# Kernel optimization log

Hardware: AMD Instinct MI355X
Metric: run time of the kernel (lower is better)

## Reference

```python
import jax, jax.numpy as jnp
import numpy as np

B = 32
C = 768
NH = 12
HD = C // NH
P = 16
IMG = 224
G = IMG // P           # 14 patches per side
NP = G * G             # 196 patches
DEPTH = 12
PRUNE = [1, 1, 1, 1, 0.5, 0.5, 0.5, 0.5, 0.5, 0.5, 0.5, 0.5]
MOM = 0.5              # momentum for global class-attention update
TRADE = 0.5            # slow-fast tradeoff for placeholder token update
SCALE = HD ** -0.5
NCLS = 1000

def _ln(x, g, b, eps=1e-6):
    mu = jnp.mean(x, -1, keepdims=True)
    var = jnp.mean((x - mu) ** 2, -1, keepdims=True)
    return (x - mu) * jax.lax.rsqrt(var + eps) * g + b

def setup_inputs():
    key = jax.random.key(0)
    ks = iter(jax.random.split(key, 40))
    def rn(shape, s=0.02):
        return jax.random.normal(next(ks), shape, jnp.float32) * s
    return {
        'x_img': jax.random.normal(next(ks), (B, 3, IMG, IMG), jnp.float32),
        'cls_token': rn((1, 1, C)),
        'pos_embed': rn((1, NP + 1, C)),
        'patch_w': rn((3 * P * P, C)),
        'patch_b': rn((C,)),
        'ln1_g': jnp.ones((DEPTH, C), jnp.float32),
        'ln1_b': jnp.zeros((DEPTH, C), jnp.float32),
        'qk_w': rn((DEPTH, C, 2 * C)),
        'qk_b': rn((DEPTH, 2 * C)),
        'v_w': rn((DEPTH, C, C)),
        'v_b': rn((DEPTH, C)),
        'proj_w': rn((DEPTH, C, C)),
        'proj_b': rn((DEPTH, C)),
        'ln2_g': jnp.ones((DEPTH, C), jnp.float32),
        'ln2_b': jnp.zeros((DEPTH, C), jnp.float32),
        'fc1_w': rn((DEPTH, C, 4 * C)),
        'fc1_b': rn((DEPTH, 4 * C)),
        'fc2_w': rn((DEPTH, 4 * C, C)),
        'fc2_b': rn((DEPTH, C)),
        'norm_g': jnp.ones((C,), jnp.float32),
        'norm_b': jnp.zeros((C,), jnp.float32),
        'head_w': rn((C, NCLS)),
        'head_b': rn((NCLS,)),
    }

def reference(x_img, cls_token, pos_embed, patch_w, patch_b, ln1_g, ln1_b,
              qk_w, qk_b, v_w, v_b, proj_w, proj_b, ln2_g, ln2_b,
              fc1_w, fc1_b, fc2_w, fc2_b, norm_g, norm_b, head_w, head_b):
    Bq = x_img.shape[0]
    # PatchEmbed: Conv2d(k=P, stride=P) == flatten each patch as (c, ph, pw) then matmul
    patches = x_img.reshape(Bq, 3, G, P, G, P).transpose(0, 2, 4, 1, 3, 5)
    patches = patches.reshape(Bq, NP, 3 * P * P)
    x = patches @ patch_w + patch_b                                   # [B,196,C]
    x = jnp.concatenate([jnp.broadcast_to(cls_token, (Bq, 1, C)), x], 1)
    x = x + pos_embed                                                 # [B,197,C]

    def block(xt, i):
        # QKAttention + VAttention + proj residual, then MlpBlock residual.
        t = _ln(xt, ln1_g[i], ln1_b[i])
        Nt = t.shape[1]
        qk = (t @ qk_w[i] + qk_b[i]).reshape(Bq, Nt, 2, NH, HD)
        q = qk[:, :, 0].transpose(0, 2, 1, 3)                         # [B,H,Nt,hd]
        k = qk[:, :, 1].transpose(0, 2, 1, 3)
        attn = jax.nn.softmax(jnp.einsum('bhnd,bhmd->bhnm', q, k) * SCALE, -1)
        v = (t @ v_w[i] + v_b[i]).reshape(Bq, Nt, NH, HD).transpose(0, 2, 1, 3)
        o = jnp.einsum('bhnm,bhmd->bhnd', attn, v).transpose(0, 2, 1, 3).reshape(Bq, Nt, C)
        xt = xt + (o @ proj_w[i] + proj_b[i])
        h = _ln(xt, ln2_g[i], ln2_b[i])
        xt = xt + (jax.nn.gelu(h @ fc1_w[i] + fc1_b[i], approximate=False) @ fc2_w[i] + fc2_b[i])
        row = attn[:, :, 0, 1:].sum(1)   # cls-attention row, summed over heads
        return xt, row

    cls_attn = None
    for i in range(DEPTH):
        if PRUNE[i] == 1:
            x, row = block(x, i)
            cls_attn = row if cls_attn is None else (1 - MOM) * cls_attn + MOM * row
        else:
            N_ = int(NP * PRUNE[i])                        # informative token count
            idx = jnp.argsort(-cls_attn, axis=1)           # sort patches by score (easy_gather)
            xp = jnp.take_along_axis(x[:, 1:], idx[:, :, None], axis=1)
            cls_attn = jnp.take_along_axis(cls_attn, idx, axis=1)
            fast = xp[:, N_:]                              # placeholder (pruned) tokens
            score = cls_attn[:, N_:]
            rep = (fast * score[:, :, None]).sum(1, keepdims=True) \
                  / score.sum(1, keepdims=True)[:, :, None]  # representative token
            xs = jnp.concatenate([x[:, :1], xp[:, :N_], rep], 1)   # [B,N_+2,C]
            xs, row = block(xs, i)
            cls_attn = jnp.concatenate(
                [(1 - MOM) * cls_attn[:, :N_] + MOM * row[:, :N_], cls_attn[:, N_:]], 1)
            fast = fast + TRADE * (xs[:, -1:] - rep)       # fast update via rep residual
            x = jnp.concatenate([xs[:, :N_ + 1], fast], 1)  # back to [B,197,C]

    x = _ln(x, norm_g, norm_b)
    return x[:, 0] @ head_w + head_b                        # [B,1000]
```

## Files before the change

kernel.cpp:

```cpp
#include <hip/hip_runtime.h>
#include <hip/hip_bf16.h>
#include <stdint.h>

#define B_ 32
#define C_ 768
#define NH_ 12
#define HD_ 64
#define NP_ 196
#define NTOK 197
#define NKEEP 98
#define NCLS_ 1000
#define MPAD 6400
#define RS_ (3 * C_)

typedef __bf16 bf16x8 __attribute__((ext_vector_type(8)));
typedef float f32x4 __attribute__((ext_vector_type(4)));

__device__ __forceinline__ float blockReduceSum256(float v) {
    __shared__ float red[4];
    const int lane = threadIdx.x & 63, w = threadIdx.x >> 6;
#pragma unroll
    for (int off = 32; off; off >>= 1) v += __shfl_down(v, off);
    __syncthreads();
    if (lane == 0) red[w] = v;
    __syncthreads();
    return red[0] + red[1] + red[2] + red[3];
}

__device__ __forceinline__ void gload16(void* lds, const void* g) {
    __builtin_amdgcn_global_load_lds(
        (const __attribute__((address_space(1))) void*)g,
        (__attribute__((address_space(3))) void*)lds,
        16, 0, 0);
}

__global__ __launch_bounds__(256) void patchify_kernel(const float* __restrict__ img,
                                                       __hip_bfloat16* __restrict__ patches)
{
    const int bp = blockIdx.x;
    const int b = bp / NP_, p = bp % NP_;
    const int gy = p / 14, gx = p % 14;
    const int tid = threadIdx.x;
#pragma unroll
    for (int j = 0; j < 3; ++j) {
        const int e = tid + j * 256;
        const int c = e >> 8, rem = e & 255, py = rem >> 4, px = rem & 15;
        patches[(size_t)bp * C_ + e] = __float2bfloat16(
            img[(((size_t)b * 3 + c) * 224 + gy * 16 + py) * 224 + gx * 16 + px]);
    }
}

__global__ __launch_bounds__(256) void assemble_x_kernel(const float* __restrict__ pemb,
                                                         const float* __restrict__ cls_tok,
                                                         const float* __restrict__ pos,
                                                         float* __restrict__ x)
{
    const int b = blockIdx.x, t = blockIdx.y, tid = threadIdx.x;
#pragma unroll
    for (int j = 0; j < 3; ++j) {
        const int c = tid + j * 256;
        const float v = (t == 0) ? cls_tok[c] : pemb[((size_t)b * NP_ + (t - 1)) * C_ + c];
        x[((size_t)b * NTOK + t) * C_ + c] = v + pos[(size_t)t * C_ + c];
    }
}

__global__ __launch_bounds__(256) void ln_kernel(const float* __restrict__ x,
                                                 const float* __restrict__ g,
                                                 const float* __restrict__ b,
                                                 __hip_bfloat16* outB, float* outF,
                                                 long long inRowStride, int nRows)
{
    const int row = (blockIdx.x << 2) + (threadIdx.x >> 6);
    const int lane = threadIdx.x & 63;
    if (row >= nRows) return;
    const float* xr = x + (size_t)row * inRowStride;
    float4 v0 = *(const float4*)(xr + (lane << 2));
    float4 v1 = *(const float4*)(xr + 256 + (lane << 2));
    float4 v2 = *(const float4*)(xr + 512 + (lane << 2));
    float s = v0.x + v0.y + v0.z + v0.w + v1.x + v1.y + v1.z + v1.w
            + v2.x + v2.y + v2.z + v2.w;
#pragma unroll
    for (int off = 1; off < 64; off <<= 1) s += __shfl_xor(s, off);
    const float mu = s * (1.f / C_);
    float q = 0.f;
    {
        float d;
        d = v0.x - mu; q += d * d; d = v0.y - mu; q += d * d;
        d = v0.z - mu; q += d * d; d = v0.w - mu; q += d * d;
        d = v1.x - mu; q += d * d; d = v1.y - mu; q += d * d;
        d = v1.z - mu; q += d * d; d = v1.w - mu; q += d * d;
        d = v2.x - mu; q += d * d; d = v2.y - mu; q += d * d;
        d = v2.z - mu; q += d * d; d = v2.w - mu; q += d * d;
    }
#pragma unroll
    for (int off = 1; off < 64; off <<= 1) q += __shfl_xor(q, off);
    const float rs = rsqrtf(q * (1.f / C_) + 1e-6f);
    const float4 vv[3] = {v0, v1, v2};
#pragma unroll
    for (int j = 0; j < 3; ++j) {
        const int cbase = (j << 8) + (lane << 2);
        const float4 gv = *(const float4*)(g + cbase);
        const float4 bv = *(const float4*)(b + cbase);
        float o0 = (vv[j].x - mu) * rs * gv.x + bv.x;
        float o1 = (vv[j].y - mu) * rs * gv.y + bv.y;
        float o2 = (vv[j].z - mu) * rs * gv.z + bv.z;
        float o3 = (vv[j].w - mu) * rs * gv.w + bv.w;
        if (outB) {
            union { unsigned short us[4]; uint2 u; } pk;
            __hip_bfloat16 h;
            h = __float2bfloat16(o0); pk.us[0] = *(unsigned short*)&h;
            h = __float2bfloat16(o1); pk.us[1] = *(unsigned short*)&h;
            h = __float2bfloat16(o2); pk.us[2] = *(unsigned short*)&h;
            h = __float2bfloat16(o3); pk.us[3] = *(unsigned short*)&h;
            *(uint2*)((unsigned short*)outB + (size_t)row * C_ + cbase) = pk.u;
        }
        if (outF) {
            float4 o; o.x = o0; o.y = o1; o.z = o2; o.w = o3;
            *(float4*)(outF + (size_t)row * C_ + cbase) = o;
        }
    }
}

__global__ __launch_bounds__(256) void transpose_bf16_kernel(const float* __restrict__ W,
                                                             __hip_bfloat16* __restrict__ Wt,
                                                             int K, int N,
                                                             long long outLstride, long long outOff)
{
    __shared__ float tile[32][33];
    const size_t loffIn = (size_t)blockIdx.z * K * N;
    const size_t loffOut = (size_t)blockIdx.z * outLstride + outOff;
    const int k0 = blockIdx.y << 5, n0 = blockIdx.x << 5;
    const int tid = threadIdx.x;
#pragma unroll
    for (int e = tid; e < 1024; e += 256) {
        const int r = e >> 5, c = e & 31;
        tile[r][c] = W[loffIn + (size_t)(k0 + r) * N + n0 + c];
    }
    __syncthreads();
#pragma unroll
    for (int e = tid; e < 1024; e += 256) {
        const int r = e >> 5, c = e & 31;
        Wt[loffOut + (size_t)(n0 + r) * K + k0 + c] = __float2bfloat16(tile[c][r]);
    }
}

__global__ __launch_bounds__(256) void concat_bias_kernel(const float* __restrict__ qk_b,
                                                          const float* __restrict__ v_b,
                                                          float* __restrict__ out)
{
    const int i = blockIdx.x * 256 + threadIdx.x;
    if (i < 12 * RS_) {
        const int l = i / RS_, c = i % RS_;
        out[i] = (c < 2 * C_) ? qk_b[l * 2 * C_ + c] : v_b[l * C_ + (c - 2 * C_)];
    }
}

template<int GELU, int OMODE>
__global__ __launch_bounds__(256) void gemm_bf16_kernel(const __hip_bfloat16* __restrict__ A,
                                                        const __hip_bfloat16* __restrict__ Bt,
                                                        const float* __restrict__ bias,
                                                        const float* __restrict__ res,
                                                        float* __restrict__ outF,
                                                        __hip_bfloat16* __restrict__ outB,
                                                        int K, int N)
{
    __shared__ __align__(16) unsigned short sLDS[4][128 * 64];
    const int tid = threadIdx.x;
    const int wv = tid >> 6, ln = tid & 63;

    const int nwg = gridDim.x * gridDim.y;
    int lid = blockIdx.y * gridDim.x + blockIdx.x;
    {
        const int q = nwg >> 3, r = nwg & 7;
        const int xcd = lid & 7, lq = lid >> 3;
        lid = (xcd < r ? xcd * (q + 1) : r * (q + 1) + (xcd - r) * q) + lq;
    }
    const int bn = (lid % gridDim.x) << 7;
    const int bm = (lid / gridDim.x) << 7;

    const int wr = wv >> 1, wc = wv & 1;
    const int ln15 = ln & 15, lhi = ln >> 4;

    const int srow = tid >> 3;
    const int gc = (tid & 7) ^ ((tid >> 3) & 7);
    const __hip_bfloat16* gA = A + (size_t)(bm + srow) * K + (gc << 3);
    const __hip_bfloat16* gB = Bt + (size_t)(bn + srow) * K + (gc << 3);

    const unsigned ldsBase =
        (unsigned)(size_t)(__attribute__((address_space(3))) unsigned short*)&sLDS[0][0];
    unsigned rowA[4], rowB[4];
#pragma unroll
    for (int m = 0; m < 4; ++m) rowA[m] = (unsigned)(((wr << 6) + (m << 4) + ln15) << 7);
#pragma unroll
    for (int n = 0; n < 4; ++n) rowB[n] = (unsigned)(((wc << 6) + (n << 4) + ln15) << 7);
    const int swk = ln15 & 7;

    f32x4 acc[4][4] = {};

    auto stage = [&](int bufA, int bufB, int k0) {
#pragma unroll
        for (int i = 0; i < 4; ++i) {
            gload16(&sLDS[bufA][(wv << 9) + (i << 11)], gA + (size_t)(i << 5) * K + k0);
            gload16(&sLDS[bufB][(wv << 9) + (i << 11)], gB + (size_t)(i << 5) * K + k0);
        }
    };
    auto compute = [&](unsigned aOff, unsigned bOff) {
#pragma unroll
        for (int kk = 0; kk < 2; ++kk) {
            const unsigned chb = (unsigned)(((((kk << 2) + lhi)) ^ swk) << 4);
            bf16x8 a[4], b[4];
#pragma unroll
            for (int m = 0; m < 4; ++m)
                asm volatile("ds_read_b128 %0, %1"
                             : "=v"(a[m]) : "v"(ldsBase + aOff + rowA[m] + chb));
#pragma unroll
            for (int n = 0; n < 4; ++n)
                asm volatile("ds_read_b128 %0, %1"
                             : "=v"(b[n]) : "v"(ldsBase + bOff + rowB[n] + chb));
            asm volatile("s_waitcnt lgkmcnt(0)" ::: "memory");
            __builtin_amdgcn_sched_barrier(0);
#pragma unroll
            for (int m = 0; m < 4; ++m)
#pragma unroll
                for (int n = 0; n < 4; ++n)
                    acc[m][n] = __builtin_amdgcn_mfma_f32_16x16x32_bf16(a[m], b[n], acc[m][n], 0, 0, 0);
        }
    };

    const int ntiles = K >> 6;
    stage(0, 1, 0);
    asm volatile("s_waitcnt vmcnt(0)" ::: "memory");
    __builtin_amdgcn_s_barrier();
    int t = 0;
    for (; t + 2 < ntiles; t += 2) {
        stage(2, 3, (t + 1) << 6);
        asm volatile("s_waitcnt vmcnt(8)" ::: "memory");
        __builtin_amdgcn_s_barrier();
        compute(0u, 16384u);
        __builtin_amdgcn_s_barrier();
        stage(0, 1, (t + 2) << 6);
        asm volatile("s_waitcnt vmcnt(8)" ::: "memory");
        __builtin_amdgcn_s_barrier();
        compute(32768u, 49152u);
        __builtin_amdgcn_s_barrier();
    }
    stage(2, 3, (ntiles - 1) << 6);
    asm volatile("s_waitcnt vmcnt(8)" ::: "memory");
    __builtin_amdgcn_s_barrier();
    compute(0u, 16384u);
    __builtin_amdgcn_s_barrier();
    asm volatile("s_waitcnt vmcnt(0)" ::: "memory");
    __builtin_amdgcn_s_barrier();
    compute(32768u, 49152u);
    __syncthreads();

    if (OMODE == 0) {
        unsigned short* sOut = &sLDS[0][0];
#pragma unroll
        for (int n = 0; n < 4; ++n) {
            const int col = (wc << 6) + (n << 4) + ln15;
            const float bv = bias[bn + col];
#pragma unroll
            for (int m = 0; m < 4; ++m) {
                const int row0 = (wr << 6) + (m << 4) + (lhi << 2);
#pragma unroll
                for (int r = 0; r < 4; ++r) {
                    float x = acc[m][n][r] + bv;
                    if (GELU) x = 0.5f * x * (1.f + erff(x * 0.70710678118654752f));
                    const __hip_bfloat16 hb = __float2bfloat16(x);
                    sOut[(row0 + r) * 128 + col] = *(const unsigned short*)&hb;
                }
            }
        }
        __syncthreads();
#pragma unroll
        for (int i = 0; i < 8; ++i) {
            const int chunk = (i << 8) + tid;
            const int row = chunk >> 4, c8 = (chunk & 15) << 3;
            *(uint4*)((unsigned short*)outB + (size_t)(bm + row) * N + bn + c8) =
                *(const uint4*)(sOut + row * 128 + c8);
        }
    } else {
#pragma unroll
        for (int n = 0; n < 4; ++n) {
            const int gcn = bn + (wc << 6) + (n << 4) + ln15;
            const float bv = bias[gcn];
#pragma unroll
            for (int m = 0; m < 4; ++m) {
                const int gr0 = bm + (wr << 6) + (m << 4) + (lhi << 2);
                f32x4 v = acc[m][n];
#pragma unroll
                for (int r = 0; r < 4; ++r) {
                    const size_t o = (size_t)(gr0 + r) * N + gcn;
                    float x = v[r] + bv;
                    if (OMODE == 1) x += res[o];
                    outF[o] = x;
                }
            }
        }
    }
}

__global__ __launch_bounds__(256) void head_kernel(const float* __restrict__ A,
                                                   const float* __restrict__ W,
                                                   const float* __restrict__ bias,
                                                   float* __restrict__ out)
{
    const int n = blockIdx.x * 256 + threadIdx.x;
    const int m = blockIdx.y;
    if (n >= NCLS_) return;
    const float* a = A + (size_t)m * C_;
    float s = 0.f;
#pragma unroll 8
    for (int k = 0; k < C_; ++k) s = fmaf(a[k], W[(size_t)k * NCLS_ + n], s);
    out[(size_t)m * NCLS_ + n] = s + bias[n];
}

template<int NT16>
__global__ __launch_bounds__(256) void attn_mfma_kernel(const __hip_bfloat16* __restrict__ qkv,
                                                        __hip_bfloat16* __restrict__ o,
                                                        float* __restrict__ attn0,
                                                        int Nt)
{
    constexpr int NPAD = NT16 * 16;
    constexpr int PSW = (((NPAD / 8) & 7) == 0) ? 7 : 3;
    constexpr int VSW = 7;
    constexpr int PROWB = NPAD * 2 + 16;
    constexpr int VROWB = (NPAD == 224) ? 528 : 272;
    __shared__ unsigned short sK[NPAD * 64 + 512];
    __shared__ unsigned short sV[32 * VROWB];

    const int bh = blockIdx.x;
    const int b = bh / NH_, h = bh % NH_;
    const int qtile = blockIdx.y;
    const int tid = threadIdx.x, ln = tid & 63, wv = tid >> 6;
    const int ln15 = ln & 15, lhi = ln >> 4;
    const __hip_bfloat16* qkbase = qkv + (size_t)b * Nt * RS_;

#pragma unroll
    for (int it = 0; it < NPAD * 8 / 256; ++it) {
        const int p = it * 256 + tid;
        int key = p >> 3;
        const int c = (p & 7) ^ (key & 7);
        if (key >= Nt) key = Nt - 1;
        unsigned short* dst = sK + (size_t)(it * 256 + (wv << 6)) * 8;
        gload16(dst, qkbase + (size_t)key * RS_ + C_ + (h << 6) + (c << 3));
    }
#pragma unroll
    for (int it = 0; it < NPAD * 8 / 256; ++it) {
        const int e = it * 256 + tid;
        const int key = e >> 3, dc = e & 7;
        union { uint4 u; unsigned short us[8]; } val;
        val.u = make_uint4(0u, 0u, 0u, 0u);
        if (key < Nt)
            val.u = *(const uint4*)(qkbase + (size_t)key * RS_ + 2 * C_ + (h << 6) + (dc << 3));
        const int kc = key >> 3, kb = (key & 7) << 1;
#pragma unroll
        for (int j = 0; j < 8; ++j) {
            const int d = (dc << 3) + j;
            *(unsigned short*)((char*)sV + d * VROWB + ((kc ^ ((d >> 3) & VSW)) << 4) + kb) = val.us[j];
        }
    }
    const int qbase = qtile * 64 + (wv << 4);
    int qrow = qbase + ln15; if (qrow >= Nt) qrow = Nt - 1;
    const __hip_bfloat16* qp = qkbase + (size_t)qrow * RS_ + (h << 6) + (lhi << 3);
    const bf16x8 qf0 = *(const bf16x8*)qp;
    const bf16x8 qf1 = *(const bf16x8*)(qp + 32);
    __syncthreads();

    f32x4 sc[NT16];
#pragma unroll
    for (int t = 0; t < NT16; ++t) {
        const int key = (t << 4) + ln15;
        const unsigned short* kr = sK + (size_t)key * 64;
        const bf16x8 k0 = *(const bf16x8*)(kr + ((lhi ^ (key & 7)) << 3));
        const bf16x8 k1 = *(const bf16x8*)(kr + (((4 + lhi) ^ (key & 7)) << 3));
        f32x4 a = {0.f, 0.f, 0.f, 0.f};
        a = __builtin_amdgcn_mfma_f32_16x16x32_bf16(k0, qf0, a, 0, 0, 0);
        a = __builtin_amdgcn_mfma_f32_16x16x32_bf16(k1, qf1, a, 0, 0, 0);
        sc[t] = a;
    }
    __syncthreads();

    float mx = -1e30f;
#pragma unroll
    for (int t = 0; t < NT16; ++t)
#pragma unroll
        for (int r = 0; r < 4; ++r) {
            const int key = (t << 4) + (lhi << 2) + r;
            const float v = (key < Nt) ? sc[t][r] * 0.125f : -1e30f;
            sc[t][r] = v;
            mx = fmaxf(mx, v);
        }
    mx = fmaxf(mx, __shfl_xor(mx, 16));
    mx = fmaxf(mx, __shfl_xor(mx, 32));
    float sum = 0.f;
#pragma unroll
    for (int t = 0; t < NT16; ++t)
#pragma unroll
        for (int r = 0; r < 4; ++r) {
            const float e = expf(sc[t][r] - mx);
            sc[t][r] = e; sum += e;
        }
    sum += __shfl_xor(sum, 16);
    sum += __shfl_xor(sum, 32);
    const float inv = 1.f / sum;

    char* Pw = (char*)sK + wv * (16 * PROWB);
    const bool isQ0 = (qtile == 0) && (wv == 0) && (ln15 == 0);
#pragma unroll
    for (int t = 0; t < NT16; ++t) {
        union { unsigned short us[4]; uint2 u2; } pk;
#pragma unroll
        for (int r = 0; r < 4; ++r) {
            const float p = sc[t][r] * inv;
            const __hip_bfloat16 hb = __float2bfloat16(p);
            pk.us[r] = *(const unsigned short*)&hb;
            if (isQ0) {
                const int key = (t << 4) + (lhi << 2) + r;
                if (key < Nt) attn0[(size_t)bh * NTOK + key] = p;
            }
        }
        const int chunk = ((t << 1) + (lhi >> 1)) ^ (ln15 & PSW);
        *(uint2*)(Pw + ln15 * PROWB + (chunk << 4) + ((lhi & 1) << 3)) = pk.u2;
    }
    __syncthreads();

    f32x4 oa[4] = {};
#pragma unroll
    for (int s = 0; s < NPAD / 32; ++s) {
        const bf16x8 pf = *(const bf16x8*)(Pw + ln15 * PROWB +
                                           ((((s << 2) + lhi) ^ (ln15 & PSW)) << 4));
#pragma unroll
        for (int n = 0; n < 4; ++n) {
            const int d = (n << 4) + ln15;
            const bf16x8 vf = *(const bf16x8*)((char*)sV + d * VROWB +
                                               ((((s << 2) + lhi) ^ ((d >> 3) & VSW)) << 4));
            oa[n] = __builtin_amdgcn_mfma_f32_16x16x32_bf16(pf, vf, oa[n], 0, 0, 0);
        }
    }
#pragma unroll
    for (int n = 0; n < 4; ++n)
#pragma unroll
        for (int r = 0; r < 4; ++r) {
            const int qq = qbase + (lhi << 2) + r;
            if (qq < Nt)
                o[((size_t)b * Nt + qq) * C_ + (h << 6) + (n << 4) + ln15] =
                    __float2bfloat16(oa[n][r]);
        }
}

__global__ __launch_bounds__(256) void row_cls_ema_kernel(const float* __restrict__ attn0,
                                                          float* __restrict__ cls, int first)
{
    const int b = blockIdx.x, t = threadIdx.x;
    if (t < NP_) {
        float s = 0.f;
#pragma unroll
        for (int h = 0; h < NH_; ++h) s += attn0[((size_t)(b * NH_ + h)) * NTOK + 1 + t];
        const int i = b * NP_ + t;
        cls[i] = first ? s : 0.5f * cls[i] + 0.5f * s;
    }
}

__global__ __launch_bounds__(256) void row_cls_prune_kernel(const float* __restrict__ attn0,
                                                            const float* __restrict__ sorted,
                                                            float* __restrict__ cls)
{
    const int b = blockIdx.x, t = threadIdx.x;
    if (t < NP_) {
        float sv = sorted[b * NP_ + t];
        if (t < NKEEP) {
            float s = 0.f;
#pragma unroll
            for (int h = 0; h < NH_; ++h) s += attn0[((size_t)(b * NH_ + h)) * NTOK + 1 + t];
            sv = 0.5f * sv + 0.5f * s;
        }
        cls[b * NP_ + t] = sv;
    }
}

__global__ __launch_bounds__(256) void rank_kernel(const float* __restrict__ cls,
                                                   int* __restrict__ idx,
                                                   float* __restrict__ sorted,
                                                   float* __restrict__ ssum)
{
    __shared__ float sv[NP_];
    const int b = blockIdx.x, t = threadIdx.x;
    if (t < NP_) sv[t] = cls[b * NP_ + t];
    __syncthreads();
    float val = 0.f; int r = NP_;
    if (t < NP_) {
        val = sv[t];
        r = 0;
        for (int j = 0; j < NP_; ++j) {
            const float vj = sv[j];
            r += (vj > val || (vj == val && j < t)) ? 1 : 0;
        }
        idx[b * NP_ + r] = t;
        sorted[b * NP_ + r] = val;
    }
    const float contrib = (t < NP_ && r >= NKEEP) ? val : 0.f;
    const float tot = blockReduceSum256(contrib);
    if (t == 0) ssum[b] = tot;
}

__global__ __launch_bounds__(256) void build_xs_kernel(const float* __restrict__ x,
                                                       const int* __restrict__ idx,
                                                       const float* __restrict__ sorted,
                                                       const float* __restrict__ ssum,
                                                       float* __restrict__ xs,
                                                       float* __restrict__ fast,
                                                       float* __restrict__ rep)
{
    const int b = blockIdx.x, t = blockIdx.y, tid = threadIdx.x;
    const float* xb = x + (size_t)b * NTOK * C_;
    if (t == 0) {
#pragma unroll
        for (int j = 0; j < 3; ++j) {
            const int c = tid + j * 256;
            xs[(size_t)b * 100 * C_ + c] = xb[c];
        }
    } else if (t <= NKEEP) {
        const int src = 1 + idx[b * NP_ + (t - 1)];
#pragma unroll
        for (int j = 0; j < 3; ++j) {
            const int c = tid + j * 256;
            xs[((size_t)b * 100 + t) * C_ + c] = xb[(size_t)src * C_ + c];
        }
    } else if (t == NKEEP + 1) {
        const float inv = 1.f / ssum[b];
        float acc0 = 0.f, acc1 = 0.f, acc2 = 0.f;
        for (int jj = 0; jj < NP_ - NKEEP; ++jj) {
            const int src = 1 + idx[b * NP_ + NKEEP + jj];
            const float wgt = sorted[b * NP_ + NKEEP + jj];
            const float* xr = xb + (size_t)src * C_;
            acc0 = fmaf(xr[tid], wgt, acc0);
            acc1 = fmaf(xr[tid + 256], wgt, acc1);
            acc2 = fmaf(xr[tid + 512], wgt, acc2);
        }
        float* xsr = xs + ((size_t)b * 100 + 99) * C_;
        float* rr = rep + (size_t)b * C_;
        xsr[tid] = acc0 * inv;       rr[tid] = acc0 * inv;
        xsr[tid + 256] = acc1 * inv; rr[tid + 256] = acc1 * inv;
        xsr[tid + 512] = acc2 * inv; rr[tid + 512] = acc2 * inv;
    } else {
        const int jf = t - (NKEEP + 2);
        const int src = 1 + idx[b * NP_ + NKEEP + jf];
#pragma unroll
        for (int j = 0; j < 3; ++j) {
            const int c = tid + j * 256;
            fast[((size_t)b * (NP_ - NKEEP) + jf) * C_ + c] = xb[(size_t)src * C_ + c];
        }
    }
}

__global__ __launch_bounds__(256) void scatter_back_kernel(const float* __restrict__ xs,
                                                           const float* __restrict__ fast,
                                                           const float* __restrict__ rep,
                                                           float* __restrict__ x)
{
    const int b = blockIdx.x, t = blockIdx.y, tid = threadIdx.x;
#pragma unroll
    for (int j = 0; j < 3; ++j) {
        const int c = tid + j * 256;
        float v;
        if (t <= NKEEP)
            v = xs[((size_t)b * 100 + t) * C_ + c];
        else
            v = fast[((size_t)b * (NP_ - NKEEP) + (t - NKEEP - 1)) * C_ + c]
                + 0.5f * (xs[((size_t)b * 100 + 99) * C_ + c] - rep[(size_t)b * C_ + c]);
        x[((size_t)b * NTOK + t) * C_ + c] = v;
    }
}

extern "C" void kernel_launch(void* const* d_in, const int* in_sizes, int n_in,
                              void* d_out, int out_size, void* d_ws, size_t ws_size,
                              hipStream_t stream)
{
    (void)in_sizes; (void)n_in; (void)out_size;
    const float* x_img   = (const float*)d_in[0];
    const float* cls_tok = (const float*)d_in[1];
    const float* pos     = (const float*)d_in[2];
    const float* patch_w = (const float*)d_in[3];
    const float* patch_b = (const float*)d_in[4];
    const float* ln1_g   = (const float*)d_in[5];
    const float* ln1_b   = (const float*)d_in[6];
    const float* qk_w    = (const float*)d_in[7];
    const float* qk_b    = (const float*)d_in[8];
    const float* v_w     = (const float*)d_in[9];
    const float* v_b     = (const float*)d_in[10];
    const float* proj_w  = (const float*)d_in[11];
    const float* proj_b  = (const float*)d_in[12];
    const float* ln2_g   = (const float*)d_in[13];
    const float* ln2_b   = (const float*)d_in[14];
    const float* fc1_w   = (const float*)d_in[15];
    const float* fc1_b   = (const float*)d_in[16];
    const float* fc2_w   = (const float*)d_in[17];
    const float* fc2_b   = (const float*)d_in[18];
    const float* norm_g  = (const float*)d_in[19];
    const float* norm_b  = (const float*)d_in[20];
    const float* head_w  = (const float*)d_in[21];
    const float* head_b  = (const float*)d_in[22];

    char* base = (char*)d_ws;
    size_t off = 0;
    auto alloc = [&](size_t bytes) -> void* {
        void* p = base + off; off = (off + bytes + 255) & ~(size_t)255; return p;
    };
    float* X    = (float*)alloc((size_t)MPAD * C_ * 4);
    __hip_bfloat16* Tb   = (__hip_bfloat16*)alloc((size_t)MPAD * C_ * 2);
    __hip_bfloat16* QKVb = (__hip_bfloat16*)alloc((size_t)MPAD * RS_ * 2);
    __hip_bfloat16* Hb   = (__hip_bfloat16*)alloc((size_t)MPAD * 4 * C_ * 2);
    float* XS   = (float*)alloc((size_t)3200 * C_ * 4);
    float* FAST = (float*)alloc((size_t)B_ * (NP_ - NKEEP) * C_ * 4);
    float* REP  = (float*)alloc((size_t)B_ * C_ * 4);
    float* ATTN0= (float*)alloc((size_t)B_ * NH_ * NTOK * 4);
    float* CLS  = (float*)alloc((size_t)B_ * NP_ * 4);
    float* SORT = (float*)alloc((size_t)B_ * NP_ * 4);
    float* SSUM = (float*)alloc((size_t)B_ * 4);
    float* T0   = (float*)alloc((size_t)B_ * C_ * 4);
    int*   IDX  = (int*)alloc((size_t)B_ * NP_ * 4);
    float* BIASQKV = (float*)alloc((size_t)12 * RS_ * 4);
    __hip_bfloat16* WTpatch = (__hip_bfloat16*)alloc((size_t)C_ * C_ * 2);
    __hip_bfloat16* WTqkv   = (__hip_bfloat16*)alloc((size_t)12 * RS_ * C_ * 2);
    __hip_bfloat16* WTproj  = (__hip_bfloat16*)alloc((size_t)12 * C_ * C_ * 2);
    __hip_bfloat16* WTfc1   = (__hip_bfloat16*)alloc((size_t)12 * C_ * 4 * C_ * 2);
    __hip_bfloat16* WTfc2   = (__hip_bfloat16*)alloc((size_t)12 * 4 * C_ * C_ * 2);
    if (off > ws_size) return;

    __hip_bfloat16* Ob    = Hb;
    __hip_bfloat16* PATCH = Hb;
    float*          PEMB  = (float*)QKVb;

    const dim3 blk(256);

    transpose_bf16_kernel<<<dim3(24, 24, 1), blk, 0, stream>>>(patch_w, WTpatch, C_, C_, (long long)C_ * C_, 0);
    transpose_bf16_kernel<<<dim3(48, 24, 12), blk, 0, stream>>>(qk_w, WTqkv, C_, 2 * C_, (long long)RS_ * C_, 0);
    transpose_bf16_kernel<<<dim3(24, 24, 12), blk, 0, stream>>>(v_w, WTqkv, C_, C_, (long long)RS_ * C_, (long long)2 * C_ * C_);
    transpose_bf16_kernel<<<dim3(24, 24, 12), blk, 0, stream>>>(proj_w, WTproj, C_, C_, (long long)C_ * C_, 0);
    transpose_bf16_kernel<<<dim3(96, 24, 12), blk, 0, stream>>>(fc1_w, WTfc1, C_, 4 * C_, (long long)4 * C_ * C_, 0);
    transpose_bf16_kernel<<<dim3(24, 96, 12), blk, 0, stream>>>(fc2_w, WTfc2, 4 * C_, C_, (long long)4 * C_ * C_, 0);
    concat_bias_kernel<<<(12 * RS_ + 255) / 256, blk, 0, stream>>>(qk_b, v_b, BIASQKV);

    auto runBlock = [&](int i, float* xb, int Nt) {
        const int M = B_ * Nt;
        const int mt = (M + 127) >> 7;
        const int qtiles = (Nt + 63) >> 6;
        ln_kernel<<<(M + 3) / 4, blk, 0, stream>>>(xb, ln1_g + i * C_, ln1_b + i * C_, Tb, nullptr, C_, M);
        gemm_bf16_kernel<0, 0><<<dim3(RS_ / 128, mt), blk, 0, stream>>>(
            Tb, WTqkv + (size_t)i * RS_ * C_, BIASQKV + (size_t)i * RS_, nullptr, nullptr, QKVb, C_, RS_);
        if (Nt == NTOK)
            attn_mfma_kernel<14><<<dim3(B_ * NH_, qtiles), blk, 0, stream>>>(QKVb, Ob, ATTN0, Nt);
        else
            attn_mfma_kernel<8><<<dim3(B_ * NH_, qtiles), blk, 0, stream>>>(QKVb, Ob, ATTN0, Nt);
        gemm_bf16_kernel<0, 1><<<dim3(6, mt), blk, 0, stream>>>(
            Ob, WTproj + (size_t)i * C_ * C_, proj_b + (size_t)i * C_, xb, xb, nullptr, C_, C_);
        ln_kernel<<<(M + 3) / 4, blk, 0, stream>>>(xb, ln2_g + i * C_, ln2_b + i * C_, Tb, nullptr, C_, M);
        gemm_bf16_kernel<1, 0><<<dim3(24, mt), blk, 0, stream>>>(
            Tb, WTfc1 + (size_t)i * C_ * 4 * C_, fc1_b + (size_t)i * 4 * C_, nullptr, nullptr, Hb, C_, 4 * C_);
        gemm_bf16_kernel<0, 1><<<dim3(6, mt), blk, 0, stream>>>(
            Hb, WTfc2 + (size_t)i * 4 * C_ * C_, fc2_b + (size_t)i * C_, xb, xb, nullptr, 4 * C_, C_);
    };

    patchify_kernel<<<B_ * NP_, blk, 0, stream>>>(x_img, PATCH);
    gemm_bf16_kernel<0, 2><<<dim3(6, 49), blk, 0, stream>>>(
        PATCH, WTpatch, patch_b, nullptr, PEMB, nullptr, C_, C_);
    assemble_x_kernel<<<dim3(B_, NTOK), blk, 0, stream>>>(PEMB, cls_tok, pos, X);

    for (int i = 0; i < 12; ++i) {
        if (i < 4) {
            runBlock(i, X, NTOK);
            row_cls_ema_kernel<<<B_, blk, 0, stream>>>(ATTN0, CLS, i == 0 ? 1 : 0);
        } else {
            rank_kernel<<<B_, blk, 0, stream>>>(CLS, IDX, SORT, SSUM);
            build_xs_kernel<<<dim3(B_, 198), blk, 0, stream>>>(X, IDX, SORT, SSUM, XS, FAST, REP);
            runBlock(i, XS, 100);
            scatter_back_kernel<<<dim3(B_, NTOK), blk, 0, stream>>>(XS, FAST, REP, X);
            row_cls_prune_kernel<<<B_, blk, 0, stream>>>(ATTN0, SORT, CLS);
        }
    }

    ln_kernel<<<8, blk, 0, stream>>>(X, norm_g, norm_b, nullptr, T0, (long long)NTOK * C_, B_);
    head_kernel<<<dim3(4, B_), blk, 0, stream>>>(T0, head_w, head_b, (float*)d_out);
}
```

Measured before the change: 2.727 ms.

## Add 128x256-tile GEMM kernel for QKV and FC1 projections

Adds a new bf16 MFMA GEMM kernel with a 128x256 output tile, where each wave computes a 64x128 sub-tile, and uses it for the wide QKV and FC1 GEMMs. The larger tile raises arithmetic intensity and cuts the number of workgroups, so the A operand is re-read from global memory less often. In exchange it uses a single LDS buffer with no double buffering, more accumulator registers per thread (32 f32x4), and fewer workgroups for the CU array to hide latency with. The epilogue is staged through LDS in two halves.

```diff
diff --git a/kernel.cpp b/kernel.cpp
--- a/kernel.cpp
+++ b/kernel.cpp
@@ -152,6 +152,99 @@
     if (i < 12 * RS_) {
         const int l = i / RS_, c = i % RS_;
         out[i] = (c < 2 * C_) ? qk_b[l * 2 * C_ + c] : v_b[l * C_ + (c - 2 * C_)];
+    }
+}
+
+template<int GELU>
+__global__ __launch_bounds__(256) void gemm_wide_kernel(const __hip_bfloat16* __restrict__ A,
+                                                        const __hip_bfloat16* __restrict__ Bt,
+                                                        const float* __restrict__ bias,
+                                                        __hip_bfloat16* __restrict__ outB,
+                                                        int K, int N)
+{
+    __shared__ __align__(16) unsigned short sMem[(128 + 256) * 64];
+    unsigned short* sA = sMem;
+    unsigned short* sB = sMem + 128 * 64;
+    const int tid = threadIdx.x;
+    const int wv = tid >> 6, ln = tid & 63;
+
+    const int nwg = gridDim.x * gridDim.y;
+    int lid = blockIdx.y * gridDim.x + blockIdx.x;
+    {
+        const int q = nwg >> 3, r = nwg & 7;
+        const int xcd = lid & 7, lq = lid >> 3;
+        lid = (xcd < r ? xcd * (q + 1) : r * (q + 1) + (xcd - r) * q) + lq;
+    }
+    const int bn = (lid % gridDim.x) << 8;
+    const int bm = (lid / gridDim.x) << 7;
+
+    const int wr = wv >> 1, wc = wv & 1;
+    const int ln15 = ln & 15, lhi = ln >> 4;
+    const int swk = ln15 & 7;
+
+    const int arow = tid >> 3;
+    const int apch = tid & 7;
+    const __hip_bfloat16* gAp = A + (size_t)(bm + arow) * K + ((apch ^ (arow & 7)) << 3);
+    const __hip_bfloat16* gBp = Bt + (size_t)(bn + arow) * K + ((apch ^ (arow & 7)) << 3);
+
+    f32x4 acc[4][8] = {};
+    for (int k0 = 0; k0 < K; k0 += 64) {
+#pragma unroll
+        for (int i = 0; i < 4; ++i)
+            gload16(sA + (size_t)(i * 256 + (wv << 6)) * 8, gAp + (size_t)(i << 5) * K + k0);
+#pragma unroll
+        for (int i = 0; i < 8; ++i)
+            gload16(sB + (size_t)(i * 256 + (wv << 6)) * 8, gBp + (size_t)(i << 5) * K + k0);
+        __syncthreads();
+#pragma unroll
+        for (int kk = 0; kk < 2; ++kk) {
+            const int ch = ((kk << 2) + lhi) ^ swk;
+            bf16x8 a[4], b[8];
+#pragma unroll
+            for (int m = 0; m < 4; ++m)
+                a[m] = *(const bf16x8*)(sA + (((wr << 6) + (m << 4) + ln15) << 6) + (ch << 3));
+#pragma unroll
+            for (int n = 0; n < 8; ++n)
+                b[n] = *(const bf16x8*)(sB + (((wc << 7) + (n << 4) + ln15) << 6) + (ch << 3));
+#pragma unroll
+            for (int m = 0; m < 4; ++m)
+#pragma unroll
+                for (int n = 0; n < 8; ++n)
+                    acc[m][n] = __builtin_amdgcn_mfma_f32_16x16x32_bf16(a[m], b[n], acc[m][n], 0, 0, 0);
+        }
+        __syncthreads();
+    }
+
+    unsigned short* sOut = sMem;
+#pragma unroll
+    for (int p = 0; p < 2; ++p) {
+        if (wc == p) {
+#pragma unroll
+            for (int n = 0; n < 8; ++n) {
+                const int coll = (n << 4) + ln15;
+                const float bv = bias[bn + (p << 7) + coll];
+#pragma unroll
+                for (int m = 0; m < 4; ++m) {
+                    const int row0 = (wr << 6) + (m << 4) + (lhi << 2);
+#pragma unroll
+                    for (int r = 0; r < 4; ++r) {
+                        float x = acc[m][n][r] + bv;
+                        if (GELU) x = 0.5f * x * (1.f + erff(x * 0.70710678118654752f));
+                        const __hip_bfloat16 hb = __float2bfloat16(x);
+                        sOut[(row0 + r) * 128 + coll] = *(const unsigned short*)&hb;
+                    }
+                }
+            }
+        }
+        __syncthreads();
+#pragma unroll
+        for (int i = 0; i < 8; ++i) {
+            const int slot = (i << 8) + tid;
+            const int row = slot >> 4, c8 = (slot & 15) << 3;
+            *(uint4*)((unsigned short*)outB + (size_t)(bm + row) * N + bn + (p << 7) + c8) =
+                *(const uint4*)(sOut + row * 128 + c8);
+        }
+        __syncthreads();
     }
 }
 
@@ -648,8 +741,8 @@
         const int mt = (M + 127) >> 7;
         const int qtiles = (Nt + 63) >> 6;
         ln_kernel<<<(M + 3) / 4, blk, 0, stream>>>(xb, ln1_g + i * C_, ln1_b + i * C_, Tb, nullptr, C_, M);
-        gemm_bf16_kernel<0, 0><<<dim3(RS_ / 128, mt), blk, 0, stream>>>(
-            Tb, WTqkv + (size_t)i * RS_ * C_, BIASQKV + (size_t)i * RS_, nullptr, nullptr, QKVb, C_, RS_);
+        gemm_wide_kernel<0><<<dim3(RS_ / 256, mt), blk, 0, stream>>>(
+            Tb, WTqkv + (size_t)i * RS_ * C_, BIASQKV + (size_t)i * RS_, QKVb, C_, RS_);
         if (Nt == NTOK)
             attn_mfma_kernel<14><<<dim3(B_ * NH_, qtiles), blk, 0, stream>>>(QKVb, Ob, ATTN0, Nt);
         else
@@ -657,8 +750,8 @@
         gemm_bf16_kernel<0, 1><<<dim3(6, mt), blk, 0, stream>>>(
             Ob, WTproj + (size_t)i * C_ * C_, proj_b + (size_t)i * C_, xb, xb, nullptr, C_, C_);
         ln_kernel<<<(M + 3) / 4, blk, 0, stream>>>(xb, ln2_g + i * C_, ln2_b + i * C_, Tb, nullptr, C_, M);
-        gemm_bf16_kernel<1, 0><<<dim3(24, mt), blk, 0, stream>>>(
-            Tb, WTfc1 + (size_t)i * C_ * 4 * C_, fc1_b + (size_t)i * 4 * C_, nullptr, nullptr, Hb, C_, 4 * C_);
+        gemm_wide_kernel<1><<<dim3((4 * C_) / 256, mt), blk, 0, stream>>>(
+            Tb, WTfc1 + (size_t)i * C_ * 4 * C_, fc1_b + (size_t)i * 4 * C_, Hb, C_, 4 * C_);
         gemm_bf16_kernel<0, 1><<<dim3(6, mt), blk, 0, stream>>>(
             Hb, WTfc2 + (size_t)i * 4 * C_ * C_, fc2_b + (size_t)i * C_, xb, xb, nullptr, 4 * C_, C_);
     };
```

Result: slower. 3.604 ms (+32.2%).

## Halve GEMM K-tile to 32 and shrink LDS to raise occupancy

Applied to the files above, without the earlier changes.

Shrinks the bf16 GEMM's K step from 64 to 32, which cuts shared memory from 64KB to 32KB per block. It also changes the LDS layout so two 32-wide rows pack into each 128-byte line with a new XOR swizzle, and sets launch_bounds to 4 blocks per CU. The aim is more resident workgroups to hide memory latency. The cost is twice as many barriers and pipeline stages per K, and less MFMA work between syncs.

```diff
diff --git a/kernel.cpp b/kernel.cpp
--- a/kernel.cpp
+++ b/kernel.cpp
@@ -156,15 +156,15 @@
 }
 
 template<int GELU, int OMODE>
-__global__ __launch_bounds__(256) void gemm_bf16_kernel(const __hip_bfloat16* __restrict__ A,
-                                                        const __hip_bfloat16* __restrict__ Bt,
-                                                        const float* __restrict__ bias,
-                                                        const float* __restrict__ res,
-                                                        float* __restrict__ outF,
-                                                        __hip_bfloat16* __restrict__ outB,
-                                                        int K, int N)
-{
-    __shared__ __align__(16) unsigned short sLDS[4][128 * 64];
+__global__ __launch_bounds__(256, 4) void gemm_bf16_kernel(const __hip_bfloat16* __restrict__ A,
+                                                           const __hip_bfloat16* __restrict__ Bt,
+                                                           const float* __restrict__ bias,
+                                                           const float* __restrict__ res,
+                                                           float* __restrict__ outF,
+                                                           __hip_bfloat16* __restrict__ outB,
+                                                           int K, int N)
+{
+    __shared__ __align__(16) unsigned short sMem[16384];
     const int tid = threadIdx.x;
     const int wv = tid >> 6, ln = tid & 63;
 
@@ -181,81 +181,89 @@
     const int wr = wv >> 1, wc = wv & 1;
     const int ln15 = ln & 15, lhi = ln >> 4;
 
-    const int srow = tid >> 3;
-    const int gc = (tid & 7) ^ ((tid >> 3) & 7);
-    const __hip_bfloat16* gA = A + (size_t)(bm + srow) * K + (gc << 3);
-    const __hip_bfloat16* gB = Bt + (size_t)(bn + srow) * K + (gc << 3);
+    int offA[2], offB[2];
+#pragma unroll
+    for (int i = 0; i < 2; ++i) {
+        const int s = (i << 8) + tid;
+        const int L = s >> 3, cp = (s & 7) ^ (L & 7);
+        offA[i] = (bm + (L << 1) + (cp >> 2)) * K + ((cp & 3) << 3);
+        offB[i] = (bn + (L << 1) + (cp >> 2)) * K + ((cp & 3) << 3);
+    }
 
     const unsigned ldsBase =
-        (unsigned)(size_t)(__attribute__((address_space(3))) unsigned short*)&sLDS[0][0];
-    unsigned rowA[4], rowB[4];
-#pragma unroll
-    for (int m = 0; m < 4; ++m) rowA[m] = (unsigned)(((wr << 6) + (m << 4) + ln15) << 7);
-#pragma unroll
-    for (int n = 0; n < 4; ++n) rowB[n] = (unsigned)(((wc << 6) + (n << 4) + ln15) << 7);
-    const int swk = ln15 & 7;
+        (unsigned)(size_t)(__attribute__((address_space(3))) unsigned short*)&sMem[0];
+    unsigned aOff[4], bOff[4];
+#pragma unroll
+    for (int m = 0; m < 4; ++m) {
+        const int r = (wr << 6) + (m << 4) + ln15;
+        const int L = r >> 1;
+        const int pc = (((r & 1) << 2) + lhi) ^ (L & 7);
+        aOff[m] = (unsigned)((L << 7) + (pc << 4));
+    }
+#pragma unroll
+    for (int n = 0; n < 4; ++n) {
+        const int r = (wc << 6) + (n << 4) + ln15;
+        const int L = r >> 1;
+        const int pc = (((r & 1) << 2) + lhi) ^ (L & 7);
+        bOff[n] = (unsigned)(8192 + (L << 7) + (pc << 4));
+    }
 
     f32x4 acc[4][4] = {};
 
-    auto stage = [&](int bufA, int bufB, int k0) {
-#pragma unroll
-        for (int i = 0; i < 4; ++i) {
-            gload16(&sLDS[bufA][(wv << 9) + (i << 11)], gA + (size_t)(i << 5) * K + k0);
-            gload16(&sLDS[bufB][(wv << 9) + (i << 11)], gB + (size_t)(i << 5) * K + k0);
-        }
+    auto stage = [&](int bufByte, int kt) {
+        const int k0 = kt << 5;
+        unsigned short* base = sMem + (bufByte >> 1);
+        gload16(base + ((0 * 256 + (wv << 6)) << 3), A + offA[0] + k0);
+        gload16(base + ((1 * 256 + (wv << 6)) << 3), A + offA[1] + k0);
+        gload16(base + 4096 + ((0 * 256 + (wv << 6)) << 3), Bt + offB[0] + k0);
+        gload16(base + 4096 + ((1 * 256 + (wv << 6)) << 3), Bt + offB[1] + k0);
     };
-    auto compute = [&](unsigned aOff, unsigned bOff) {
-#pragma unroll
-        for (int kk = 0; kk < 2; ++kk) {
-            const unsigned chb = (unsigned)(((((kk << 2) + lhi)) ^ swk) << 4);
-            bf16x8 a[4], b[4];
-#pragma unroll
-            for (int m = 0; m < 4; ++m)
-                asm volatile("ds_read_b128 %0, %1"
-                             : "=v"(a[m]) : "v"(ldsBase + aOff + rowA[m] + chb));
+    auto compute = [&](unsigned bufOff) {
+        bf16x8 a[4], b[4];
+#pragma unroll
+        for (int m = 0; m < 4; ++m)
+            asm volatile("ds_read_b128 %0, %1" : "=v"(a[m]) : "v"(ldsBase + bufOff + aOff[m]));
+#pragma unroll
+        for (int n = 0; n < 4; ++n)
+            asm volatile("ds_read_b128 %0, %1" : "=v"(b[n]) : "v"(ldsBase + bufOff + bOff[n]));
+        asm volatile("s_waitcnt lgkmcnt(0)" ::: "memory");
+        __builtin_amdgcn_sched_barrier(0);
+#pragma unroll
+        for (int m = 0; m < 4; ++m)
 #pragma unroll
             for (int n = 0; n < 4; ++n)
-                asm volatile("ds_read_b128 %0, %1"
-                             : "=v"(b[n]) : "v"(ldsBase + bOff + rowB[n] + chb));
-            asm volatile("s_waitcnt lgkmcnt(0)" ::: "memory");
-            __builtin_amdgcn_sched_barrier(0);
-#pragma unroll
-            for (int m = 0; m < 4; ++m)
-#pragma unroll
-                for (int n = 0; n < 4; ++n)
-                    acc[m][n] = __builtin_amdgcn_mfma_f32_16x16x32_bf16(a[m], b[n], acc[m][n], 0, 0, 0);
-        }
+                acc[m][n] = __builtin_amdgcn_mfma_f32_16x16x32_bf16(a[m], b[n], acc[m][n], 0, 0, 0);
     };
 
-    const int ntiles = K >> 6;
-    stage(0, 1, 0);
+    const int ntiles = K >> 5;
+    stage(0, 0);
     asm volatile("s_waitcnt vmcnt(0)" ::: "memory");
     __builtin_amdgcn_s_barrier();
     int t = 0;
     for (; t + 2 < ntiles; t += 2) {
-        stage(2, 3, (t + 1) << 6);
-        asm volatile("s_waitcnt vmcnt(8)" ::: "memory");
+        stage(16384, t + 1);
+        asm volatile("s_waitcnt vmcnt(4)" ::: "memory");
         __builtin_amdgcn_s_barrier();
-        compute(0u, 16384u);
+        compute(0u);
         __builtin_amdgcn_s_barrier();
-        stage(0, 1, (t + 2) << 6);
-        asm volatile("s_waitcnt vmcnt(8)" ::: "memory");
+        stage(0, t + 2);
+        asm volatile("s_waitcnt vmcnt(4)" ::: "memory");
         __builtin_amdgcn_s_barrier();
-        compute(32768u, 49152u);
+        compute(16384u);
         __builtin_amdgcn_s_barrier();
     }
-    stage(2, 3, (ntiles - 1) << 6);
-    asm volatile("s_waitcnt vmcnt(8)" ::: "memory");
+    stage(16384, ntiles - 1);
+    asm volatile("s_waitcnt vmcnt(4)" ::: "memory");
     __builtin_amdgcn_s_barrier();
-    compute(0u, 16384u);
+    compute(0u);
     __builtin_amdgcn_s_barrier();
     asm volatile("s_waitcnt vmcnt(0)" ::: "memory");
     __builtin_amdgcn_s_barrier();
-    compute(32768u, 49152u);
+    compute(16384u);
     __syncthreads();
 
     if (OMODE == 0) {
-        unsigned short* sOut = &sLDS[0][0];
+        unsigned short* sOut = sMem;
 #pragma unroll
         for (int n = 0; n < 4; ++n) {
             const int col = (wc << 6) + (n << 4) + ln15;
```

Measured after the change: 2.575 ms. 5.6% less time.
